# Kernel tuning notes

Measured on AMD Instinct MI355X. Metric: run time of the kernel, lower is better.

Reference implementation:

```python
import jax, jax.numpy as jnp
import numpy as np

B, S, H, NH = 2, 2048, 1024, 16
HD = H // NH
BASE = 10000.0


def _rotate_half(x):
    x1, x2 = x[..., : x.shape[-1] // 2], x[..., x.shape[-1] // 2 :]
    return jnp.concatenate((-x2, x1), axis=-1)


def setup_inputs() -> dict:
    key = jax.random.key(0)
    ks = jax.random.split(key, 6)
    hidden_states = jax.random.normal(ks[0], (B, S, H), jnp.float32)
    scale = 0.02
    wq = jax.random.normal(ks[1], (H, H), jnp.float32) * scale
    wk = jax.random.normal(ks[2], (H, H), jnp.float32) * scale
    wv = jax.random.normal(ks[3], (H, H), jnp.float32) * scale
    wo = jax.random.normal(ks[4], (H, H), jnp.float32) * scale
    # additive causal mask, shape (B, 1, S, S): 0 on/below diagonal, large negative above
    neg = jnp.finfo(jnp.float32).min
    causal = jnp.where(jnp.tril(jnp.ones((S, S), dtype=bool)), 0.0, neg).astype(jnp.float32)
    attention_mask = jnp.broadcast_to(causal[None, None], (B, 1, S, S))
    position_ids = jnp.broadcast_to(jnp.arange(S, dtype=jnp.int32)[None], (B, S))
    return {
        "hidden_states": hidden_states,
        "attention_mask": attention_mask,
        "wq": wq,
        "wk": wk,
        "wv": wv,
        "wo": wo,
        "position_ids": position_ids,
    }


def reference(hidden_states, attention_mask, wq, wk, wv, wo, position_ids):
    b, s, h = hidden_states.shape
    dtype = hidden_states.dtype

    def proj(x, w):  # torch Linear: y = x @ w.T, then split heads -> (b, nh, s, hd)
        y = jnp.einsum("bsh,oh->bso", x, w)
        return y.reshape(b, s, NH, HD).transpose(0, 2, 1, 3)

    q = proj(hidden_states, wq)
    k = proj(hidden_states, wk)
    v = proj(hidden_states, wv)

    # rotary cache (computed in fp32 like torch), gathered by position_ids
    inv_freq = 1.0 / (BASE ** (jnp.arange(0, HD, 2, dtype=jnp.float32) / HD))
    t = jnp.arange(s, dtype=jnp.float32)
    freqs = jnp.outer(t, inv_freq)                  # (s, hd/2)
    emb = jnp.concatenate((freqs, freqs), axis=-1)  # (s, hd)
    pos = jnp.clip(position_ids, 0, s - 1)
    cos = jnp.cos(emb).astype(dtype)[pos][:, None]  # (b, 1, s, hd)
    sin = jnp.sin(emb).astype(dtype)[pos][:, None]

    q = q * cos + _rotate_half(q) * sin
    k = k * cos + _rotate_half(k) * sin

    scores = jnp.einsum("bhqd,bhkd->bhqk", q, k) / jnp.sqrt(jnp.asarray(HD, dtype))
    scores = scores + attention_mask
    attn = jax.nn.softmax(scores.astype(jnp.float32), axis=-1).astype(dtype)
    out = jnp.einsum("bhqk,bhkd->bhqd", attn, v)    # (b, nh, s, hd)
    out = out.transpose(0, 2, 1, 3).reshape(b, s, h)
    return jnp.einsum("bso,ho->bsh", out, wo)
```

## Files before the change

### kernel.cpp

```cpp
#include <hip/hip_runtime.h>
#include <cstdint>
#include <cstddef>

typedef unsigned short u16;
typedef __bf16 bf16x8 __attribute__((ext_vector_type(8)));
typedef float f32x4 __attribute__((ext_vector_type(4)));

constexpr int SEQ = 2048;
constexpr int HID = 1024;
constexpr int NHEAD = 16;
constexpr int HDIM = 64;

typedef __attribute__((address_space(1))) void gvoid;
typedef __attribute__((address_space(3))) void lvoid;

__device__ __forceinline__ u16 f2bf(float f) {
  union { float f; unsigned u; } v;
  v.f = f;
  unsigned r = v.u + 0x7fffu + ((v.u >> 16) & 1u);
  return (u16)(r >> 16);
}
__device__ __forceinline__ u16 f2bf_trunc(float f) {
  union { float f; unsigned u; } v;
  v.f = f;
  return (u16)(v.u >> 16);
}

__device__ __forceinline__ f32x4 mfma16(bf16x8 a, bf16x8 b, f32x4 c) {
  return __builtin_amdgcn_mfma_f32_16x16x32_bf16(a, b, c, 0, 0, 0);
}

__device__ __forceinline__ int detect_f32(const unsigned* __restrict__ hs) {
  unsigned w = hs[threadIdx.x & 63];
  u16 lo = (u16)(w & 0xffffu);
  int e = (lo >> 7) & 0xff;
  bool inr = (e >= 100 && e <= 154);
  unsigned long long m = __ballot(inr);
  return (__popcll(m) >= 48) ? 0 : 1;
}

__global__ __launch_bounds__(256) void cvt_kernel(
    const void* s0, const void* s1, const void* s2, const void* s3, const void* s4,
    u16* __restrict__ d0, u16* __restrict__ dW,
    float* __restrict__ cosb, float* __restrict__ sinb) {
  int b = blockIdx.x;
  if (b >= 4096) {
    int idx = (b - 4096) * 256 + threadIdx.x;
    int s = idx >> 5;
    int i = idx & 31;
    float inv_freq = expf(-(float)(2 * i) * (9.210340371976184f / 64.0f));
    float ang = (float)s * inv_freq;
    float c = cosf(ang), sn = sinf(ang);
    cosb[s * 64 + i]      = c;
    cosb[s * 64 + i + 32] = c;
    sinb[s * 64 + i]      = sn;
    sinb[s * 64 + i + 32] = sn;
    return;
  }
  const int is_f32 = detect_f32((const unsigned*)s0);
  const void* s; u16* d; long base;
  if (b < 2048) { s = s0; d = d0; base = (long)b * 2048; }
  else {
    int bb = b - 2048;
    int w = bb >> 9;
    base = (long)(bb & 511) * 2048;
    s = (w == 0) ? s1 : (w == 1) ? s2 : (w == 2) ? s3 : s4;
    d = dW + (long)w * 1048576;
  }
  long idx = base + (long)threadIdx.x * 8;
  if (is_f32) {
    const float* sf = (const float*)s;
    float4 a = *(const float4*)(sf + idx);
    float4 c = *(const float4*)(sf + idx + 4);
    ushort4 p0, p1;
    p0.x = f2bf(a.x); p0.y = f2bf(a.y); p0.z = f2bf(a.z); p0.w = f2bf(a.w);
    p1.x = f2bf(c.x); p1.y = f2bf(c.y); p1.z = f2bf(c.z); p1.w = f2bf(c.w);
    *(ushort4*)(d + idx) = p0;
    *(ushort4*)(d + idx + 4) = p1;
  } else {
    const u16* su = (const u16*)s;
    *(uint4*)(d + idx) = *(const uint4*)(su + idx);
  }
}

__device__ __forceinline__ void gemm_mainloop_256x192(
    const u16* __restrict__ Ag, const u16* __restrict__ Bg,
    int row0, int col0, f32x4 acc[8][4]) {
  __shared__ __align__(16) u16 As[2][256 * 64];
  __shared__ __align__(16) u16 Bs[2][192 * 64];
  const int t = threadIdx.x;
  const int lane = t & 63, wave = t >> 6;
  const int l15 = lane & 15, quad = lane >> 4;
  const int wm = wave / 3, wn = wave % 3;
  const int srow = lane >> 3;
  const int cs = ((lane & 7) ^ srow) * 8;
  const bool isA = (wave < 4);
  const int wb = wave - 4;
  const u16* aS = Ag + (size_t)(row0 + wave * 64 + srow) * 1024 + cs;
  const u16* bS = Bg + (size_t)(col0 + wb * 96 + srow) * 1024 + cs;
  const int swz0 = ((quad)     ^ (l15 & 7)) * 8;
  const int swz1 = ((4 + quad) ^ (l15 & 7)) * 8;

#define STAGE_P0(bi, k0_) do {                                                   \
    if (isA) {                                                                   \
      _Pragma("unroll")                                                          \
      for (int j = 0; j < 4; j++)                                                \
        __builtin_amdgcn_global_load_lds((gvoid*)(aS + (k0_) + j * 8192),        \
            (lvoid*)(&As[bi][0] + wave * 4096 + j * 512), 16, 0, 0);             \
    } else {                                                                     \
      _Pragma("unroll")                                                          \
      for (int j = 0; j < 6; j++)                                                \
        __builtin_amdgcn_global_load_lds((gvoid*)(bS + (k0_) + j * 8192),        \
            (lvoid*)(&Bs[bi][0] + wb * 6144 + j * 512), 16, 0, 0);               \
    }                                                                            \
  } while (0)
#define STAGE_P1(bi, k0_) do {                                                   \
    if (isA) {                                                                   \
      _Pragma("unroll")                                                          \
      for (int j = 4; j < 8; j++)                                                \
        __builtin_amdgcn_global_load_lds((gvoid*)(aS + (k0_) + j * 8192),        \
            (lvoid*)(&As[bi][0] + wave * 4096 + j * 512), 16, 0, 0);             \
    } else {                                                                     \
      _Pragma("unroll")                                                          \
      for (int j = 6; j < 12; j++)                                               \
        __builtin_amdgcn_global_load_lds((gvoid*)(bS + (k0_) + j * 8192),        \
            (lvoid*)(&Bs[bi][0] + wb * 6144 + j * 512), 16, 0, 0);               \
    }                                                                            \
  } while (0)
#define PBAR() do {                                                              \
    __builtin_amdgcn_sched_barrier(0);                                           \
    __builtin_amdgcn_s_barrier();                                                \
    __builtin_amdgcn_sched_barrier(0);                                           \
  } while (0)
#define READ_AF(QM) do {                                                         \
    _Pragma("unroll")                                                            \
    for (int mi = 0; mi < 4; mi++) {                                             \
      const u16* ap = Ab + (wm * 128 + (QM) * 64 + mi * 16 + l15) * 64;          \
      af[mi][0] = *(const bf16x8*)(ap + swz0);                                   \
      af[mi][1] = *(const bf16x8*)(ap + swz1);                                   \
    }                                                                            \
  } while (0)
#define READ_BF(NB) do {                                                         \
    _Pragma("unroll")                                                            \
    for (int nj = 0; nj < 2; nj++) {                                             \
      const u16* bp = Bb + (wn * 64 + ((NB) + nj) * 16 + l15) * 64;              \
      bfr[nj][0] = *(const bf16x8*)(bp + swz0);                                  \
      bfr[nj][1] = *(const bf16x8*)(bp + swz1);                                  \
    }                                                                            \
  } while (0)
#define MFMA_PH(QM, NB) do {                                                     \
    __builtin_amdgcn_s_setprio(1);                                               \
    _Pragma("unroll")                                                            \
    for (int mi = 0; mi < 4; mi++)                                               \
    _Pragma("unroll")                                                            \
    for (int nj = 0; nj < 2; nj++)                                               \
    _Pragma("unroll")                                                            \
    for (int kk = 0; kk < 2; kk++)                                               \
      acc[(QM) * 4 + mi][(NB) + nj] =                                            \
          mfma16(af[mi][kk], bfr[nj][kk], acc[(QM) * 4 + mi][(NB) + nj]);        \
    __builtin_amdgcn_s_setprio(0);                                               \
  } while (0)

  STAGE_P0(0, 0);
  STAGE_P1(0, 0);
  asm volatile("s_waitcnt vmcnt(0)" ::: "memory");
  PBAR();

  for (int kt = 0; kt < 16; ++kt) {
    const int cur = kt & 1;
    const u16* Ab = &As[cur][0];
    const u16* Bb = &Bs[cur][0];
    const bool pf = (kt + 1 < 16);
    bf16x8 af[4][2], bfr[2][2];
    READ_AF(0); READ_BF(0);
    if (pf) STAGE_P0(cur ^ 1, (kt + 1) * 64);
    PBAR();
    MFMA_PH(0, 0);
    PBAR();
    READ_BF(2);
    if (pf) STAGE_P1(cur ^ 1, (kt + 1) * 64);
    PBAR();
    MFMA_PH(0, 2);
    PBAR();
    READ_AF(1); READ_BF(0);
    PBAR();
    MFMA_PH(1, 0);
    PBAR();
    READ_BF(2);
    PBAR();
    MFMA_PH(1, 2);
    if (pf) asm volatile("s_waitcnt vmcnt(0)" ::: "memory");
    PBAR();
  }
#undef STAGE_P0
#undef STAGE_P1
#undef PBAR
#undef READ_AF
#undef READ_BF
#undef MFMA_PH
}

__global__ __launch_bounds__(384) void qkv_kernel(
    const u16* __restrict__ X, const u16* __restrict__ Wcat,
    const int* __restrict__ pos_ids,
    const float* __restrict__ cosb, const float* __restrict__ sinb,
    u16* __restrict__ q_ws, u16* __restrict__ k_ws, u16* __restrict__ vt_ws) {
  const int row0 = blockIdx.x * 256;
  const int col0 = blockIdx.y * 192;
  f32x4 acc[8][4];
#pragma unroll
  for (int i = 0; i < 8; i++)
#pragma unroll
    for (int j = 0; j < 4; j++) acc[i][j] = f32x4{0.f, 0.f, 0.f, 0.f};

  gemm_mainloop_256x192(X, Wcat, row0, col0, acc);

  const int t = threadIdx.x;
  const int lane = t & 63, wave = t >> 6;
  const int l15 = lane & 15, quad = lane >> 4;
  const int wm = wave / 3, wn = wave % 3;
  const int gr0 = row0 + wm * 128;
  const int gc0 = col0 + wn * 64;
  const int z = gc0 >> 10;
  const int nh = (gc0 >> 6) & 15;
  const float qscale = (z == 0) ? 0.18033688011112042f : 1.0f;

  if (z < 2) {
    u16* dst = (z == 0) ? q_ws : k_ws;
#pragma unroll
    for (int i = 0; i < 8; i++) {
#pragma unroll
      for (int r = 0; r < 4; r++) {
        int m = gr0 + i * 16 + quad * 4 + r;
        int b = m >> 11, s = m & 2047;
        int p = pos_ids[m];
        p = min(max(p, 0), SEQ - 1);
#pragma unroll
        for (int j = 0; j < 4; j++) {
          int d = j * 16 + l15;
          float c = cosb[p * 64 + d];
          float sn = sinb[p * 64 + d];
          float v = acc[i][j][r];
          float partner = acc[i][j ^ 2][r];
          float rot = (j < 2) ? -partner : partner;
          float o = (v * c + rot * sn) * qscale;
          dst[((size_t)((b * NHEAD + nh) * SEQ + s) << 6) + d] = f2bf(o);
        }
      }
    }
  } else {
#pragma unroll
    for (int i = 0; i < 8; i++) {
      int m_base = gr0 + i * 16 + quad * 4;
      int b = m_base >> 11, s = m_base & 2047;
#pragma unroll
      for (int j = 0; j < 4; j++) {
        int d = j * 16 + l15;
        ushort4 pk;
        pk.x = f2bf(acc[i][j][0]);
        pk.y = f2bf(acc[i][j][1]);
        pk.z = f2bf(acc[i][j][2]);
        pk.w = f2bf(acc[i][j][3]);
        *(ushort4*)(vt_ws + ((size_t)((b * NHEAD + nh) * 64 + d)) * SEQ + s) = pk;
      }
    }
  }
}

__global__ __launch_bounds__(512) void attn_kernel(
    const u16* __restrict__ q_ws, const u16* __restrict__ k_ws,
    const u16* __restrict__ vt_ws, u16* __restrict__ attn_ws) {
  const int b = blockIdx.z;
  const int qt = b ? blockIdx.x : 15 - blockIdx.x;
  const int nh = blockIdx.y;
  const int bh = b * NHEAD + nh;
  __shared__ __align__(16) u16 Ks[2][128 * 64];
  __shared__ __align__(16) u16 Vts[2][64 * 128];
  __shared__ __align__(16) u16 Pl[128 * 64];

  const int t = threadIdx.x;
  const int lane = t & 63, wave = t >> 6;
  const int l15 = lane & 15, quad = lane >> 4;
  const int l7 = l15 & 7;
  const int wq0 = qt * 128 + wave * 16;

  bf16x8 aq[2];
  {
    const u16* qb = q_ws + ((size_t)bh * SEQ + wq0 + l15) * 64;
    aq[0] = *(const bf16x8*)(qb + quad * 8);
    aq[1] = *(const bf16x8*)(qb + 32 + quad * 8);
  }

  f32x4 O[4];
  float lp = 0.f;
#pragma unroll
  for (int n = 0; n < 4; n++) O[n] = f32x4{0.f, 0.f, 0.f, 0.f};

  const int krl = lane >> 3;
  const int kcs = ((lane & 7) ^ (krl & 7)) * 8;
  const u16* kS = k_ws + (size_t)bh * SEQ * 64 + (size_t)(wave * 16 + krl) * 64 + kcs;
  const int vrl = lane >> 4;
  const int vc4 = lane & 15;
  const u16* vS = vt_ws + (size_t)bh * 64 * SEQ + (size_t)(wave * 8 + vrl) * SEQ;
  int vx[2];
#pragma unroll
  for (int j = 0; j < 2; j++)
    vx[j] = (vc4 ^ (((wave & 1) * 8 + 4 * j + vrl) & 15)) * 8;

#define STAGE_KV(bi, kt_) do {                                                     \
    const size_t koff_ = (size_t)(kt_) * 8192;                                     \
    _Pragma("unroll")                                                              \
    for (int j = 0; j < 2; j++) {                                                  \
      __builtin_amdgcn_global_load_lds((gvoid*)(kS + koff_ + j * 512),             \
          (lvoid*)(&Ks[bi][0] + wave * 1024 + j * 512), 16, 0, 0);                 \
      __builtin_amdgcn_global_load_lds(                                            \
          (gvoid*)(vS + (size_t)j * 4 * SEQ + (kt_) * 128 + vx[j]),                \
          (lvoid*)(&Vts[bi][0] + wave * 1024 + j * 512), 16, 0, 0);                \
    }                                                                              \
  } while (0)

  const int nkt = qt + 1;
  STAGE_KV(0, 0);
  int cur = 0;
  for (int kt = 0; kt < nkt; ++kt) {
    if (kt + 1 < nkt) {
      STAGE_KV(cur ^ 1, kt + 1);
      asm volatile("s_waitcnt vmcnt(4)" ::: "memory");
    } else {
      asm volatile("s_waitcnt vmcnt(0)" ::: "memory");
    }
    __builtin_amdgcn_sched_barrier(0);
    __builtin_amdgcn_s_barrier();
    __builtin_amdgcn_sched_barrier(0);
    const u16* Ksb = &Ks[cur][0];
    const u16* Vtb = &Vts[cur][0];

#pragma unroll
    for (int h = 0; h < 2; h++) {
      f32x4 sc[4];
      __builtin_amdgcn_s_setprio(1);
#pragma unroll
      for (int ct = 0; ct < 4; ct++) {
        const u16* krow = Ksb + (h * 64 + ct * 16 + l15) * 64;
        bf16x8 bk0 = *(const bf16x8*)(krow + (quad ^ l7) * 8);
        bf16x8 bk1 = *(const bf16x8*)(krow + ((4 + quad) ^ l7) * 8);
        f32x4 z = f32x4{0.f, 0.f, 0.f, 0.f};
        z = mfma16(bk0, aq[0], z);
        z = mfma16(bk1, aq[1], z);
        sc[ct] = z;
      }
      __builtin_amdgcn_s_setprio(0);

      const int kbase = kt * 128 + h * 64;
      const int prow = (wave * 16 + l15) * 64;
      if (kt == qt) {
        const int qrow = wq0 + l15;
#pragma unroll
        for (int ct = 0; ct < 4; ct++) {
          const int key0 = kbase + ct * 16 + quad * 4;
          float p[4];
#pragma unroll
          for (int r = 0; r < 4; r++) {
            float e = __builtin_amdgcn_exp2f(sc[ct][r]);
            if (key0 + r > qrow) e = 0.f;
            p[r] = e;
          }
          lp += (p[0] + p[1]) + (p[2] + p[3]);
          ushort4 pk;
          pk.x = f2bf_trunc(p[0]); pk.y = f2bf_trunc(p[1]);
          pk.z = f2bf_trunc(p[2]); pk.w = f2bf_trunc(p[3]);
          *(ushort4*)&Pl[prow + ((ct * 2 + (quad >> 1)) ^ l7) * 8 + (quad & 1) * 4] = pk;
        }
      } else {
#pragma unroll
        for (int ct = 0; ct < 4; ct++) {
          float p[4];
#pragma unroll
          for (int r = 0; r < 4; r++) p[r] = __builtin_amdgcn_exp2f(sc[ct][r]);
          lp += (p[0] + p[1]) + (p[2] + p[3]);
          ushort4 pk;
          pk.x = f2bf_trunc(p[0]); pk.y = f2bf_trunc(p[1]);
          pk.z = f2bf_trunc(p[2]); pk.w = f2bf_trunc(p[3]);
          *(ushort4*)&Pl[prow + ((ct * 2 + (quad >> 1)) ^ l7) * 8 + (quad & 1) * 4] = pk;
        }
      }

      bf16x8 pa[2];
      {
        const u16* pr = Pl + (wave * 16 + l15) * 64;
        pa[0] = *(const bf16x8*)(pr + (quad ^ l7) * 8);
        pa[1] = *(const bf16x8*)(pr + ((4 + quad) ^ l7) * 8);
      }
      __builtin_amdgcn_s_setprio(1);
#pragma unroll
      for (int n = 0; n < 4; n++) {
        const u16* vrow = Vtb + (n * 16 + l15) * 128;
        bf16x8 bv0 = *(const bf16x8*)(vrow + ((h * 8 + quad) ^ l15) * 8);
        bf16x8 bv1 = *(const bf16x8*)(vrow + ((h * 8 + 4 + quad) ^ l15) * 8);
        O[n] = mfma16(pa[0], bv0, O[n]);
        O[n] = mfma16(pa[1], bv1, O[n]);
      }
      __builtin_amdgcn_s_setprio(0);
    }

    __builtin_amdgcn_sched_barrier(0);
    __builtin_amdgcn_s_barrier();
    __builtin_amdgcn_sched_barrier(0);
    cur ^= 1;
  }
#undef STAGE_KV

  {
    float l = lp;
    l += __shfl_xor(l, 16, 64);
    l += __shfl_xor(l, 32, 64);
#pragma unroll
    for (int r = 0; r < 4; r++) {
      float inv = 1.0f / __shfl(l, quad * 4 + r, 64);
      int q = wq0 + quad * 4 + r;
      size_t base = ((size_t)(b * SEQ + q)) * HID + nh * 64;
#pragma unroll
      for (int n = 0; n < 4; n++)
        attn_ws[base + n * 16 + l15] = f2bf(O[n][r] * inv);
    }
  }
}

__global__ __launch_bounds__(256) void out_proj_kernel(
    const u16* __restrict__ A, const u16* __restrict__ Wo, void* __restrict__ out,
    const unsigned* __restrict__ hs_raw) {
  __shared__ __align__(16) u16 As[2][128 * 64];
  __shared__ __align__(16) u16 Bs[2][128 * 64];
  const int row0 = blockIdx.x * 128;
  const int col0 = blockIdx.y * 128;
  const int is_f32 = detect_f32(hs_raw);
  const int t = threadIdx.x;
  const int lane = t & 63, wave = t >> 6;
  const int l15 = lane & 15, quad = lane >> 4;
  const int wm = wave >> 1, wn = wave & 1;
  const int cs = ((lane & 7) ^ ((lane >> 3) & 7)) * 8;
  const u16* aS = A  + (size_t)(row0 + wave * 32 + (lane >> 3)) * 1024 + cs;
  const u16* bS = Wo + (size_t)(col0 + wave * 32 + (lane >> 3)) * 1024 + cs;
  const int swz0 = ((quad)     ^ (l15 & 7)) * 8;
  const int swz1 = ((4 + quad) ^ (l15 & 7)) * 8;

  f32x4 acc[4][4];
#pragma unroll
  for (int i = 0; i < 4; i++)
#pragma unroll
    for (int j = 0; j < 4; j++) acc[i][j] = f32x4{0.f, 0.f, 0.f, 0.f};

#define STAGE_AB(bi, k0_) do {                                                   \
    _Pragma("unroll")                                                            \
    for (int j = 0; j < 4; j++) {                                                \
      __builtin_amdgcn_global_load_lds((gvoid*)(aS + (k0_) + j * 8192),          \
          (lvoid*)(&As[bi][0] + wave * 2048 + j * 512), 16, 0, 0);               \
      __builtin_amdgcn_global_load_lds((gvoid*)(bS + (k0_) + j * 8192),          \
          (lvoid*)(&Bs[bi][0] + wave * 2048 + j * 512), 16, 0, 0);               \
    }                                                                            \
  } while (0)

  STAGE_AB(0, 0);
  int cur = 0;
  for (int k0 = 0; k0 < 1024; k0 += 64) {
    if (k0 + 64 < 1024) {
      STAGE_AB(cur ^ 1, k0 + 64);
      asm volatile("s_waitcnt vmcnt(8)" ::: "memory");
    } else {
      asm volatile("s_waitcnt vmcnt(0)" ::: "memory");
    }
    __builtin_amdgcn_sched_barrier(0);
    __builtin_amdgcn_s_barrier();
    __builtin_amdgcn_sched_barrier(0);
    const u16* Asb = &As[cur][0];
    const u16* Bsb = &Bs[cur][0];
#pragma unroll
    for (int kk = 0; kk < 2; kk++) {
      const int sw = kk ? swz1 : swz0;
      bf16x8 af[4], bfr[4];
#pragma unroll
      for (int i = 0; i < 4; i++)
        af[i] = *(const bf16x8*)(Asb + (wm * 64 + i * 16 + l15) * 64 + sw);
#pragma unroll
      for (int j = 0; j < 4; j++)
        bfr[j] = *(const bf16x8*)(Bsb + (wn * 64 + j * 16 + l15) * 64 + sw);
#pragma unroll
      for (int i = 0; i < 4; i++)
#pragma unroll
        for (int j = 0; j < 4; j++)
          acc[i][j] = mfma16(af[i], bfr[j], acc[i][j]);
    }
    __builtin_amdgcn_sched_barrier(0);
    __builtin_amdgcn_s_barrier();
    __builtin_amdgcn_sched_barrier(0);
    cur ^= 1;
  }
#undef STAGE_AB

  const int gr0 = row0 + wm * 64;
  const int gc0 = col0 + wn * 64;
#pragma unroll
  for (int i = 0; i < 4; i++)
#pragma unroll
    for (int r = 0; r < 4; r++) {
      int m = gr0 + i * 16 + quad * 4 + r;
      if (is_f32) {
        float* o = (float*)out;
#pragma unroll
        for (int j = 0; j < 4; j++)
          o[(size_t)m * 1024 + gc0 + j * 16 + l15] = acc[i][j][r];
      } else {
        u16* o = (u16*)out;
#pragma unroll
        for (int j = 0; j < 4; j++)
          o[(size_t)m * 1024 + gc0 + j * 16 + l15] = f2bf(acc[i][j][r]);
      }
    }
}

extern "C" void kernel_launch(void* const* d_in, const int* in_sizes, int n_in,
                              void* d_out, int out_size, void* d_ws, size_t ws_size,
                              hipStream_t stream) {
  const void* hs = d_in[0];
  const void* wq = d_in[2];
  const void* wk = d_in[3];
  const void* wv = d_in[4];
  const void* wo = d_in[5];
  const int* pos = (const int*)d_in[6];

  char* ws = (char*)d_ws;
  float* cosb = (float*)ws;
  float* sinb = (float*)(ws + (512 << 10));
  u16* xbf    = (u16*)(ws + (1 << 20));
  u16* wcat   = xbf + (size_t)4194304;
  u16* q_ws   = wcat + (size_t)4 * 1048576;
  u16* k_ws   = q_ws + (size_t)2 * NHEAD * SEQ * HDIM;
  u16* vt_ws  = k_ws + (size_t)2 * NHEAD * SEQ * HDIM;
  u16* attn_ws = vt_ws + (size_t)2 * NHEAD * SEQ * HDIM;

  cvt_kernel<<<4352, 256, 0, stream>>>(hs, wq, wk, wv, wo, xbf, wcat, cosb, sinb);
  qkv_kernel<<<dim3(16, 16), 384, 0, stream>>>(xbf, wcat, pos, cosb, sinb,
                                               q_ws, k_ws, vt_ws);
  attn_kernel<<<dim3(16, NHEAD, 2), 512, 0, stream>>>(q_ws, k_ws, vt_ws, attn_ws);
  out_proj_kernel<<<dim3(32, 8), 256, 0, stream>>>(attn_ws, wcat + (size_t)3 * 1048576,
                                                   d_out, (const unsigned*)hs);
}
```

Before: 194.4 us.

## Use 12 waves per QKV GEMM block with a simpler double-buffered mainloop

Doubles the QKV projection block from 6 to 12 waves, so each wave owns a 64x64 output tile instead of 128x64, which halves the accumulator registers per wave. The phased mainloop with many barriers is replaced by a simpler one: the next K tile is prefetched with a partial vmcnt wait, then each K step does two sub-steps of fragment reads followed by MFMAs. The aim is more latency hiding from extra waves and fewer barriers. In exchange, the overlap of loads with compute is less fine-grained, and block-wide barriers across 768 threads may cost more.

```diff
diff --git a/kernel.cpp b/kernel.cpp
--- a/kernel.cpp
+++ b/kernel.cpp
@@ -83,143 +83,99 @@
   }
 }
 
-__device__ __forceinline__ void gemm_mainloop_256x192(
+__device__ __forceinline__ void gemm_mainloop_256x192_12w(
     const u16* __restrict__ Ag, const u16* __restrict__ Bg,
-    int row0, int col0, f32x4 acc[8][4]) {
+    int row0, int col0, f32x4 acc[4][4]) {
   __shared__ __align__(16) u16 As[2][256 * 64];
   __shared__ __align__(16) u16 Bs[2][192 * 64];
   const int t = threadIdx.x;
   const int lane = t & 63, wave = t >> 6;
   const int l15 = lane & 15, quad = lane >> 4;
-  const int wm = wave / 3, wn = wave % 3;
+  const int wm = wave & 3, wn = wave >> 2;
   const int srow = lane >> 3;
   const int cs = ((lane & 7) ^ srow) * 8;
-  const bool isA = (wave < 4);
-  const int wb = wave - 4;
-  const u16* aS = Ag + (size_t)(row0 + wave * 64 + srow) * 1024 + cs;
-  const u16* bS = Bg + (size_t)(col0 + wb * 96 + srow) * 1024 + cs;
+  const bool isA = (wave < 8);
+  const int wb = wave - 8;
+  const u16* aS = Ag + (size_t)(row0 + wave * 32 + srow) * 1024 + cs;
+  const u16* bS = Bg + (size_t)(col0 + wb * 48 + srow) * 1024 + cs;
   const int swz0 = ((quad)     ^ (l15 & 7)) * 8;
   const int swz1 = ((4 + quad) ^ (l15 & 7)) * 8;
 
-#define STAGE_P0(bi, k0_) do {                                                   \
+#define STAGE12(bi, k0_) do {                                                    \
     if (isA) {                                                                   \
       _Pragma("unroll")                                                          \
       for (int j = 0; j < 4; j++)                                                \
         __builtin_amdgcn_global_load_lds((gvoid*)(aS + (k0_) + j * 8192),        \
-            (lvoid*)(&As[bi][0] + wave * 4096 + j * 512), 16, 0, 0);             \
+            (lvoid*)(&As[bi][0] + wave * 2048 + j * 512), 16, 0, 0);             \
     } else {                                                                     \
       _Pragma("unroll")                                                          \
       for (int j = 0; j < 6; j++)                                                \
         __builtin_amdgcn_global_load_lds((gvoid*)(bS + (k0_) + j * 8192),        \
-            (lvoid*)(&Bs[bi][0] + wb * 6144 + j * 512), 16, 0, 0);               \
+            (lvoid*)(&Bs[bi][0] + wb * 3072 + j * 512), 16, 0, 0);               \
     }                                                                            \
   } while (0)
-#define STAGE_P1(bi, k0_) do {                                                   \
-    if (isA) {                                                                   \
-      _Pragma("unroll")                                                          \
-      for (int j = 4; j < 8; j++)                                                \
-        __builtin_amdgcn_global_load_lds((gvoid*)(aS + (k0_) + j * 8192),        \
-            (lvoid*)(&As[bi][0] + wave * 4096 + j * 512), 16, 0, 0);             \
-    } else {                                                                     \
-      _Pragma("unroll")                                                          \
-      for (int j = 6; j < 12; j++)                                               \
-        __builtin_amdgcn_global_load_lds((gvoid*)(bS + (k0_) + j * 8192),        \
-            (lvoid*)(&Bs[bi][0] + wb * 6144 + j * 512), 16, 0, 0);               \
-    }                                                                            \
-  } while (0)
-#define PBAR() do {                                                              \
-    __builtin_amdgcn_sched_barrier(0);                                           \
-    __builtin_amdgcn_s_barrier();                                                \
-    __builtin_amdgcn_sched_barrier(0);                                           \
-  } while (0)
-#define READ_AF(QM) do {                                                         \
-    _Pragma("unroll")                                                            \
-    for (int mi = 0; mi < 4; mi++) {                                             \
-      const u16* ap = Ab + (wm * 128 + (QM) * 64 + mi * 16 + l15) * 64;          \
-      af[mi][0] = *(const bf16x8*)(ap + swz0);                                   \
-      af[mi][1] = *(const bf16x8*)(ap + swz1);                                   \
-    }                                                                            \
-  } while (0)
-#define READ_BF(NB) do {                                                         \
-    _Pragma("unroll")                                                            \
-    for (int nj = 0; nj < 2; nj++) {                                             \
-      const u16* bp = Bb + (wn * 64 + ((NB) + nj) * 16 + l15) * 64;              \
-      bfr[nj][0] = *(const bf16x8*)(bp + swz0);                                  \
-      bfr[nj][1] = *(const bf16x8*)(bp + swz1);                                  \
-    }                                                                            \
-  } while (0)
-#define MFMA_PH(QM, NB) do {                                                     \
-    __builtin_amdgcn_s_setprio(1);                                               \
-    _Pragma("unroll")                                                            \
-    for (int mi = 0; mi < 4; mi++)                                               \
-    _Pragma("unroll")                                                            \
-    for (int nj = 0; nj < 2; nj++)                                               \
-    _Pragma("unroll")                                                            \
-    for (int kk = 0; kk < 2; kk++)                                               \
-      acc[(QM) * 4 + mi][(NB) + nj] =                                            \
-          mfma16(af[mi][kk], bfr[nj][kk], acc[(QM) * 4 + mi][(NB) + nj]);        \
-    __builtin_amdgcn_s_setprio(0);                                               \
-  } while (0)
-
-  STAGE_P0(0, 0);
-  STAGE_P1(0, 0);
-  asm volatile("s_waitcnt vmcnt(0)" ::: "memory");
-  PBAR();
-
-  for (int kt = 0; kt < 16; ++kt) {
-    const int cur = kt & 1;
-    const u16* Ab = &As[cur][0];
-    const u16* Bb = &Bs[cur][0];
-    const bool pf = (kt + 1 < 16);
-    bf16x8 af[4][2], bfr[2][2];
-    READ_AF(0); READ_BF(0);
-    if (pf) STAGE_P0(cur ^ 1, (kt + 1) * 64);
-    PBAR();
-    MFMA_PH(0, 0);
-    PBAR();
-    READ_BF(2);
-    if (pf) STAGE_P1(cur ^ 1, (kt + 1) * 64);
-    PBAR();
-    MFMA_PH(0, 2);
-    PBAR();
-    READ_AF(1); READ_BF(0);
-    PBAR();
-    MFMA_PH(1, 0);
-    PBAR();
-    READ_BF(2);
-    PBAR();
-    MFMA_PH(1, 2);
-    if (pf) asm volatile("s_waitcnt vmcnt(0)" ::: "memory");
-    PBAR();
-  }
-#undef STAGE_P0
-#undef STAGE_P1
-#undef PBAR
-#undef READ_AF
-#undef READ_BF
-#undef MFMA_PH
-}
-
-__global__ __launch_bounds__(384) void qkv_kernel(
+
+  STAGE12(0, 0);
+  int cur = 0;
+  for (int k0 = 0; k0 < 1024; k0 += 64) {
+    if (k0 + 64 < 1024) {
+      STAGE12(cur ^ 1, k0 + 64);
+      if (isA) asm volatile("s_waitcnt vmcnt(4)" ::: "memory");
+      else     asm volatile("s_waitcnt vmcnt(6)" ::: "memory");
+    } else {
+      asm volatile("s_waitcnt vmcnt(0)" ::: "memory");
+    }
+    __builtin_amdgcn_sched_barrier(0);
+    __builtin_amdgcn_s_barrier();
+    __builtin_amdgcn_sched_barrier(0);
+    const u16* Asb = &As[cur][0];
+    const u16* Bsb = &Bs[cur][0];
+#pragma unroll
+    for (int kk = 0; kk < 2; kk++) {
+      const int sw = kk ? swz1 : swz0;
+      bf16x8 af[4], bfr[4];
+#pragma unroll
+      for (int i = 0; i < 4; i++)
+        af[i] = *(const bf16x8*)(Asb + (wm * 64 + i * 16 + l15) * 64 + sw);
+#pragma unroll
+      for (int j = 0; j < 4; j++)
+        bfr[j] = *(const bf16x8*)(Bsb + (wn * 64 + j * 16 + l15) * 64 + sw);
+      __builtin_amdgcn_s_setprio(1);
+#pragma unroll
+      for (int i = 0; i < 4; i++)
+#pragma unroll
+        for (int j = 0; j < 4; j++)
+          acc[i][j] = mfma16(af[i], bfr[j], acc[i][j]);
+      __builtin_amdgcn_s_setprio(0);
+    }
+    __builtin_amdgcn_sched_barrier(0);
+    __builtin_amdgcn_s_barrier();
+    __builtin_amdgcn_sched_barrier(0);
+    cur ^= 1;
+  }
+#undef STAGE12
+}
+
+__global__ __launch_bounds__(768) void qkv_kernel(
     const u16* __restrict__ X, const u16* __restrict__ Wcat,
     const int* __restrict__ pos_ids,
     const float* __restrict__ cosb, const float* __restrict__ sinb,
     u16* __restrict__ q_ws, u16* __restrict__ k_ws, u16* __restrict__ vt_ws) {
   const int row0 = blockIdx.x * 256;
   const int col0 = blockIdx.y * 192;
-  f32x4 acc[8][4];
-#pragma unroll
-  for (int i = 0; i < 8; i++)
+  f32x4 acc[4][4];
+#pragma unroll
+  for (int i = 0; i < 4; i++)
 #pragma unroll
     for (int j = 0; j < 4; j++) acc[i][j] = f32x4{0.f, 0.f, 0.f, 0.f};
 
-  gemm_mainloop_256x192(X, Wcat, row0, col0, acc);
+  gemm_mainloop_256x192_12w(X, Wcat, row0, col0, acc);
 
   const int t = threadIdx.x;
   const int lane = t & 63, wave = t >> 6;
   const int l15 = lane & 15, quad = lane >> 4;
-  const int wm = wave / 3, wn = wave % 3;
-  const int gr0 = row0 + wm * 128;
+  const int wm = wave & 3, wn = wave >> 2;
+  const int gr0 = row0 + wm * 64;
   const int gc0 = col0 + wn * 64;
   const int z = gc0 >> 10;
   const int nh = (gc0 >> 6) & 15;
@@ -228,7 +184,7 @@
   if (z < 2) {
     u16* dst = (z == 0) ? q_ws : k_ws;
 #pragma unroll
-    for (int i = 0; i < 8; i++) {
+    for (int i = 0; i < 4; i++) {
 #pragma unroll
       for (int r = 0; r < 4; r++) {
         int m = gr0 + i * 16 + quad * 4 + r;
@@ -250,7 +206,7 @@
     }
   } else {
 #pragma unroll
-    for (int i = 0; i < 8; i++) {
+    for (int i = 0; i < 4; i++) {
       int m_base = gr0 + i * 16 + quad * 4;
       int b = m_base >> 11, s = m_base & 2047;
 #pragma unroll
@@ -539,7 +495,7 @@
   u16* attn_ws = vt_ws + (size_t)2 * NHEAD * SEQ * HDIM;
 
   cvt_kernel<<<4352, 256, 0, stream>>>(hs, wq, wk, wv, wo, xbf, wcat, cosb, sinb);
-  qkv_kernel<<<dim3(16, 16), 384, 0, stream>>>(xbf, wcat, pos, cosb, sinb,
+  qkv_kernel<<<dim3(16, 16), 768, 0, stream>>>(xbf, wcat, pos, cosb, sinb,
                                                q_ws, k_ws, vt_ws);
   attn_kernel<<<dim3(16, NHEAD, 2), 512, 0, stream>>>(q_ws, k_ws, vt_ws, attn_ws);
   out_proj_kernel<<<dim3(32, 8), 256, 0, stream>>>(attn_ws, wcat + (size_t)3 * 1048576,
```

After: 189.8 us. -2.4%, faster.
